# Kernel optimization log

Measured on AMD Instinct MI355X. Metric: run time of the kernel, lower is better.

The kernel has to match this reference:

```python
import jax, jax.numpy as jnp
import numpy as np

SIZE = 256  # matrix dimension n; input vector length = n*(n-1)/2
BATCH = 512

# strictly-lower indices in the same row-major (i, j<i) order as the module's l_indices
_ROWS, _COLS = np.tril_indices(SIZE, k=-1)


def setup_inputs() -> dict:
    key = jax.random.key(0)
    m = SIZE * (SIZE - 1) // 2
    # z entries are partial-correlation-like values, must lie in (-1, 1)
    vec = jax.random.uniform(key, (BATCH, m), dtype=jnp.float32, minval=-0.99, maxval=0.99)
    return {"vec": vec}


def reference(vec):
    B = vec.shape[0]
    n = SIZE
    # scatter vector into strictly-lower triangle: (B, n, n)
    z = jnp.zeros((B, n, n), dtype=vec.dtype).at[:, _ROWS, _COLS].set(vec)
    signs = jnp.sign(z)
    signs = jnp.where(signs == 0, jnp.asarray(1.0, vec.dtype), signs)
    z2 = z * z

    row_idx = jnp.arange(n)  # (n,)

    def step(rowsum, inp):
        # rowsum: (B, n) running sum of x_squared over already-built columns, per row
        j, z2_col = inp  # z2_col: (B, n) = z^2[:, :, j]
        base = z2_col * (1.0 - rowsum)           # lower entries (rows > j)
        col = jnp.where(row_idx[None, :] == j, jnp.asarray(1.0, vec.dtype),
                        jnp.where(row_idx[None, :] < j, jnp.asarray(0.0, vec.dtype), base))
        return rowsum + col, col

    z2_cols = jnp.moveaxis(z2, -1, 0)  # (n_col, B, n_row)
    _, x2_cols = jax.lax.scan(step, jnp.zeros((B, n), dtype=vec.dtype),
                              (jnp.arange(n), z2_cols))
    # x2_cols: (n_col, B, n_row) -> (B, n_row, n_col)
    x2 = jnp.moveaxis(x2_cols, 0, -1)
    return jnp.sqrt(x2) * signs
```

## Files before the change

kernel.cpp:

```cpp
#include <hip/hip_runtime.h>


#define SIZE 256
#define BATCH 512
#define M (SIZE * (SIZE - 1) / 2)

__global__ __launch_bounds__(256) void chol_from_z_kernel(
    const float* __restrict__ vec, float* __restrict__ out) {
    const int lane = threadIdx.x & 63;
    const int wave = (blockIdx.x * blockDim.x + threadIdx.x) >> 6;
    const int b = wave >> 8;
    const int i = wave & 255;

    const size_t row_off = (size_t)b * M + ((size_t)i * (size_t)(i - 1)) / 2;
    const float* __restrict__ s = vec + row_off;
    float* __restrict__ dst = out + (((size_t)b * SIZE) + i) * SIZE;

    const int L = i;
    float carry = 1.0f;

    #pragma unroll
    for (int c = 0; c < 4; ++c) {
        const int j = c * 64 + lane;
        if (c * 64 > i) {
            dst[j] = 0.0f;
            continue;
        }
        float z = 0.0f;
        if (j < L) z = s[j];
        float t = 1.0f - z * z;

        float p = t;
        #pragma unroll
        for (int d = 1; d < 64; d <<= 1) {
            float v = __shfl_up(p, d, 64);
            if (lane >= d) p *= v;
        }
        float excl = __shfl_up(p, 1, 64);
        if (lane == 0) excl = 1.0f;
        const float P = carry * excl;

        float x;
        if (j < L)       x = z * sqrtf(P);
        else if (j == i) x = 1.0f;
        else             x = 0.0f;
        dst[j] = x;

        carry *= __shfl(p, 63, 64);
    }
}

extern "C" void kernel_launch(void* const* d_in, const int* in_sizes, int n_in,
                              void* d_out, int out_size, void* d_ws, size_t ws_size,
                              hipStream_t stream) {
    const float* vec = (const float*)d_in[0];
    float* out = (float*)d_out;
    const int n_waves = BATCH * SIZE;
    const int blocks = n_waves / 4;
    chol_from_z_kernel<<<blocks, 256, 0, stream>>>(vec, out);
}
```

Before: 210.1 us.

## Give each lane four consecutive columns with a single wave scan and float4 stores

```diff
diff --git a/kernel.cpp b/kernel.cpp
--- a/kernel.cpp
+++ b/kernel.cpp
@@ -14,40 +14,39 @@
 
     const size_t row_off = (size_t)b * M + ((size_t)i * (size_t)(i - 1)) / 2;
     const float* __restrict__ s = vec + row_off;
-    float* __restrict__ dst = out + (((size_t)b * SIZE) + i) * SIZE;
+    float* __restrict__ dst = out + (((size_t)b << 8) + (size_t)i) * SIZE;
 
     const int L = i;
-    float carry = 1.0f;
+    const int j0 = lane << 2;
 
+    float z0 = 0.f, z1 = 0.f, z2 = 0.f, z3 = 0.f;
+    if (j0     < L) z0 = s[j0];
+    if (j0 + 1 < L) z1 = s[j0 + 1];
+    if (j0 + 2 < L) z2 = s[j0 + 2];
+    if (j0 + 3 < L) z3 = s[j0 + 3];
+
+    const float t0 = 1.f - z0 * z0;
+    const float t1 = 1.f - z1 * z1;
+    const float t2 = 1.f - z2 * z2;
+    const float t3 = 1.f - z3 * z3;
+    float local = t0 * t1 * t2 * t3;
+
+    float p = local;
     #pragma unroll
-    for (int c = 0; c < 4; ++c) {
-        const int j = c * 64 + lane;
-        if (c * 64 > i) {
-            dst[j] = 0.0f;
-            continue;
-        }
-        float z = 0.0f;
-        if (j < L) z = s[j];
-        float t = 1.0f - z * z;
+    for (int d = 1; d < 64; d <<= 1) {
+        float v = __shfl_up(p, d, 64);
+        if (lane >= d) p *= v;
+    }
+    float run = __shfl_up(p, 1, 64);
+    if (lane == 0) run = 1.f;
 
-        float p = t;
-        #pragma unroll
-        for (int d = 1; d < 64; d <<= 1) {
-            float v = __shfl_up(p, d, 64);
-            if (lane >= d) p *= v;
-        }
-        float excl = __shfl_up(p, 1, 64);
-        if (lane == 0) excl = 1.0f;
-        const float P = carry * excl;
+    float4 o;
+    o.x = (j0     < L) ? z0 * sqrtf(run) : ((j0     == i) ? 1.f : 0.f); run *= t0;
+    o.y = (j0 + 1 < L) ? z1 * sqrtf(run) : ((j0 + 1 == i) ? 1.f : 0.f); run *= t1;
+    o.z = (j0 + 2 < L) ? z2 * sqrtf(run) : ((j0 + 2 == i) ? 1.f : 0.f); run *= t2;
+    o.w = (j0 + 3 < L) ? z3 * sqrtf(run) : ((j0 + 3 == i) ? 1.f : 0.f);
 
-        float x;
-        if (j < L)       x = z * sqrtf(P);
-        else if (j == i) x = 1.0f;
-        else             x = 0.0f;
-        dst[j] = x;
-
-        carry *= __shfl(p, 63, 64);
-    }
+    *(float4*)(dst + j0) = o;
 }
 
 extern "C" void kernel_launch(void* const* d_in, const int* in_sizes, int n_in,
```

Measured after the change: 183.0 us. -12.9%, faster.
